# Kernel optimization log

Hardware: AMD Instinct MI355X
Metric: run time of the kernel (lower is better)

The kernel has to match this reference:

```python
import jax, jax.numpy as jnp
import numpy as np

D_MODEL = 1024
NUM_HEADS = 16
D_K = D_MODEL // NUM_HEADS


def setup_inputs() -> dict:
    key = jax.random.key(0)
    ks = jax.random.split(key, 12)
    B, S, D = 2, 2048, D_MODEL
    s = 1.0 / np.sqrt(D)
    inp = {
        "Q": jax.random.normal(ks[0], (B, S, D), jnp.float32),
        "K": jax.random.normal(ks[1], (B, S, D), jnp.float32),
        "V": jax.random.normal(ks[2], (B, S, D), jnp.float32),
        "Wq": jax.random.normal(ks[3], (D, D), jnp.float32) * s,
        "bq": jax.random.normal(ks[4], (D,), jnp.float32) * s,
        "Wk": jax.random.normal(ks[5], (D, D), jnp.float32) * s,
        "bk": jax.random.normal(ks[6], (D,), jnp.float32) * s,
        "Wv": jax.random.normal(ks[7], (D, D), jnp.float32) * s,
        "bv": jax.random.normal(ks[8], (D,), jnp.float32) * s,
        "Wo": jax.random.normal(ks[9], (D, D), jnp.float32) * s,
        "bo": jax.random.normal(ks[10], (D,), jnp.float32) * s,
    }
    return inp


def _split_heads(x, B, S):
    # [B, S, D] -> [B, H, S, d_k]
    return x.reshape(B, S, NUM_HEADS, D_K).transpose(0, 2, 1, 3)


def reference(Q, K, V, Wq, bq, Wk, bk, Wv, bv, Wo, bo):
    B, S, D = Q.shape
    # torch nn.Linear: y = x @ W.T + b
    q = _split_heads(Q @ Wq.T + bq, B, S)
    k = _split_heads(K @ Wk.T + bk, B, S)
    v = _split_heads(V @ Wv.T + bv, B, S)
    scale = 1.0 / np.sqrt(D_K).astype(np.float32)
    # [B, H, S, S] attention scores (materialized, as in the original)
    scores = jnp.einsum('bhqd,bhkd->bhqk', q, k) * scale
    probs = jax.nn.softmax(scores, axis=-1)
    out = jnp.einsum('bhqk,bhkd->bhqd', probs, v)
    out = out.transpose(0, 2, 1, 3).reshape(B, S, D)
    return out @ Wo.T + bo
```

## Files before the change

### kernel.cpp

```cpp
#include <hip/hip_runtime.h>
#include <hip/hip_bf16.h>

#define S_LEN   2048
#define NHEADS  16
#define DKH     64
#define DMODEL  1024
#define NBATCH  2

typedef __bf16 bf16x8 __attribute__((ext_vector_type(8)));
typedef __bf16 bf16x4 __attribute__((ext_vector_type(4)));
typedef float  f32x4  __attribute__((ext_vector_type(4)));

typedef __attribute__((address_space(3))) void       lds_void;
typedef const __attribute__((address_space(1))) void glob_void;

__device__ __forceinline__ void glds16(const void* g, void* l) {
    __builtin_amdgcn_global_load_lds((glob_void*)g, (lds_void*)l, 16, 0, 0);
}

struct CvtArgs {
    const float* src[7];
    __bf16*      dst[7];
    int          n[7];
};

__global__ __launch_bounds__(256)
void cvt_all_k(CvtArgs a)
{
    const int t = blockIdx.y;
    const size_t i = ((size_t)blockIdx.x * 256 + threadIdx.x) * 8;
    if ((int)i >= a.n[t]) return;
    const float* s = a.src[t];
    f32x4 lo = *(const f32x4*)(s + i);
    f32x4 hi = *(const f32x4*)(s + i + 4);
    bf16x8 r;
#pragma unroll
    for (int k = 0; k < 4; ++k) { r[k] = (__bf16)lo[k]; r[4 + k] = (__bf16)hi[k]; }
    *(bf16x8*)(a.dst[t] + i) = r;
}

__device__ __forceinline__ void gemm_core(
    const __bf16* __restrict__ A, const __bf16* __restrict__ W,
    int m0, int n0, int K,
    __bf16 (*As)[32], __bf16 (*Ws)[32], f32x4 acc[4][4])
{
    const int tid  = threadIdx.x;
    const int lane = tid & 63;
    const int wv   = tid >> 6;
    const int l15  = lane & 15;
    const int quad = lane >> 4;
    const int wm   = wv >> 1;
    const int wn   = wv & 1;
    const int grow = lane >> 2;
    const int gcol = (lane & 3) * 8;

    const __bf16* ag0 = A + (size_t)(m0 + wv * 32 + grow) * K + gcol;
    const __bf16* ag1 = A + (size_t)(m0 + wv * 32 + 16 + grow) * K + gcol;
    const __bf16* wg0 = W + (size_t)(n0 + wv * 32 + grow) * K + gcol;
    const __bf16* wg1 = W + (size_t)(n0 + wv * 32 + 16 + grow) * K + gcol;
    void* al0 = &As[wv * 32][0];
    void* al1 = &As[wv * 32 + 16][0];
    void* wl0 = &Ws[wv * 32][0];
    void* wl1 = &Ws[wv * 32 + 16][0];

    for (int k0 = 0;;) {
        __syncthreads();
        glds16(ag0 + k0, al0);
        glds16(ag1 + k0, al1);
        glds16(wg0 + k0, wl0);
        glds16(wg1 + k0, wl1);
        __syncthreads();

        bf16x8 af[4], wf[4];
#pragma unroll
        for (int i = 0; i < 4; ++i)
            af[i] = *(const bf16x8*)&As[wm * 64 + i * 16 + l15][quad * 8];
#pragma unroll
        for (int j = 0; j < 4; ++j)
            wf[j] = *(const bf16x8*)&Ws[wn * 64 + j * 16 + l15][quad * 8];
#pragma unroll
        for (int i = 0; i < 4; ++i)
#pragma unroll
            for (int j = 0; j < 4; ++j)
                acc[i][j] = __builtin_amdgcn_mfma_f32_16x16x32_bf16(af[i], wf[j], acc[i][j], 0, 0, 0);

        k0 += 32;
        if (k0 >= K) break;
    }
}

struct GArgs {
    const __bf16* A[3];
    const __bf16* W[3];
    const float*  bias[3];
    __bf16*       out[3];
};

__global__ __launch_bounds__(256)
void gemm_qkv(GArgs g, int z_off)
{
    __shared__ __align__(16) __bf16 As[128][32];
    __shared__ __align__(16) __bf16 Ws[128][32];

    const int fid = blockIdx.x;
    const int z   = (fid >> 8) + z_off;
    const int f8  = fid & 255;
    int m0, n0;
    if (z == 2) { m0 = (f8 & 7) * 128;  n0 = (f8 >> 3) * 128; }
    else        { m0 = (f8 & 31) * 128; n0 = (f8 >> 5) * 128; }

    f32x4 acc[4][4];
#pragma unroll
    for (int i = 0; i < 4; ++i)
#pragma unroll
        for (int j = 0; j < 4; ++j) acc[i][j] = (f32x4){0.f, 0.f, 0.f, 0.f};

    gemm_core(g.A[z], g.W[z], m0, n0, DMODEL, As, Ws, acc);

    const int lane = threadIdx.x & 63;
    const int wv   = threadIdx.x >> 6;
    const int l15  = lane & 15;
    const int quad = lane >> 4;
    const int wm   = wv >> 1;
    const int wn   = wv & 1;
    const float* bias = g.bias[z];
    __bf16* out = g.out[z];
    const float oscale = (z == 0) ? 0.125f * 1.44269504088896f : 1.0f;

#pragma unroll
    for (int j = 0; j < 4; ++j) {
        const int col = n0 + wn * 64 + j * 16 + l15;
        const float bcol = (z == 2) ? 0.f : bias[col];
#pragma unroll
        for (int i = 0; i < 4; ++i) {
#pragma unroll
            for (int r = 0; r < 4; ++r) {
                const int row = m0 + wm * 64 + i * 16 + quad * 4 + r;
                size_t idx;
                float v = acc[i][j][r];
                if (z == 2) {
                    const int h = row >> 6, d = row & (DKH - 1);
                    const int b = col >> 11, s = col & (S_LEN - 1);
                    v += bias[row];
                    idx = ((size_t)(b * NHEADS + h) * DKH + d) * S_LEN + s;
                } else {
                    const int b = row >> 11, s = row & (S_LEN - 1);
                    const int h = col >> 6, d = col & (DKH - 1);
                    v = (v + bcol) * oscale;
                    idx = ((size_t)(b * NHEADS + h) * S_LEN + s) * DKH + d;
                }
                out[idx] = (__bf16)v;
            }
        }
    }
}

__global__ __launch_bounds__(256)
void gemm_out(const __bf16* __restrict__ A, const __bf16* __restrict__ W,
              const float* __restrict__ bias, float* __restrict__ out)
{
    __shared__ __align__(16) __bf16 As[128][32];
    __shared__ __align__(16) __bf16 Ws[128][32];

    const int fid = blockIdx.x;
    const int m0 = (fid & 31) * 128;
    const int n0 = (fid >> 5) * 128;

    f32x4 acc[4][4];
#pragma unroll
    for (int i = 0; i < 4; ++i)
#pragma unroll
        for (int j = 0; j < 4; ++j) acc[i][j] = (f32x4){0.f, 0.f, 0.f, 0.f};

    gemm_core(A, W, m0, n0, DMODEL, As, Ws, acc);

    const int lane = threadIdx.x & 63;
    const int wv   = threadIdx.x >> 6;
    const int l15  = lane & 15;
    const int quad = lane >> 4;
    const int wm   = wv >> 1;
    const int wn   = wv & 1;

#pragma unroll
    for (int j = 0; j < 4; ++j) {
        const int col = n0 + wn * 64 + j * 16 + l15;
        const float bv = bias[col];
#pragma unroll
        for (int i = 0; i < 4; ++i)
#pragma unroll
            for (int r = 0; r < 4; ++r) {
                const int row = m0 + wm * 64 + i * 16 + quad * 4 + r;
                out[(size_t)row * DMODEL + col] = acc[i][j][r] + bv;
            }
    }
}

__global__ __launch_bounds__(256, 2)
void attn_k(const __bf16* __restrict__ Qh, const __bf16* __restrict__ Kh,
            const __bf16* __restrict__ VhT, __bf16* __restrict__ out,
            float* __restrict__ opart, float* __restrict__ lpart, int ksplit)
{
    __shared__ __align__(16) __bf16 Ks[2][128][64];
    __shared__ __align__(16) __bf16 Vs[64][136];

    const int tid  = threadIdx.x;
    const int lane = tid & 63;
    const int wv   = tid >> 6;
    const int l15  = lane & 15;
    const int quad = lane >> 4;

    const int fid  = blockIdx.x;
    const int x    = fid & 7;
    const int j    = fid >> 3;
    const int bh   = x * 4 + (j & 3);
    const int rest = j >> 2;
    const int q0   = (rest & 7) * 256;
    const int kh   = rest >> 3;
    const int klen = S_LEN / ksplit;
    const int kbeg = kh * klen;
    const int b  = bh >> 4;
    const int h  = bh & (NHEADS - 1);

    const __bf16* Q  = Qh  + (size_t)bh * S_LEN * DKH;
    const __bf16* Kp = Kh  + (size_t)bh * S_LEN * DKH;
    const __bf16* Vt = VhT + (size_t)bh * DKH * S_LEN;

    const int qr0 = q0 + wv * 64 + l15;
    bf16x8 qf[4][2];
#pragma unroll
    for (int s = 0; s < 4; ++s) {
        qf[s][0] = *(const bf16x8*)(Q + (size_t)(qr0 + s * 16) * DKH + quad * 8);
        qf[s][1] = *(const bf16x8*)(Q + (size_t)(qr0 + s * 16) * DKH + quad * 8 + 32);
    }

    const int srow = lane >> 3;
    const int scol = ((lane & 7) ^ srow) << 3;
    char* const ksbase = (char*)&Ks[0][0][0];
    const __bf16* kg[4];
    int kdst[4];
#pragma unroll
    for (int i = 0; i < 4; ++i) {
        const int r = wv * 8 + i * 32 + srow;
        kg[i]   = Kp + (size_t)r * DKH + scol;
        kdst[i] = (wv * 8 + i * 32) * 128;
    }

    const int vrow = tid >> 2;
    const int vc0  = (tid & 3) * 32;
    const __bf16* vst = Vt + (size_t)vrow * S_LEN + vc0;

    f32x4 o[4][4];
#pragma unroll
    for (int s = 0; s < 4; ++s)
#pragma unroll
        for (int jt = 0; jt < 4; ++jt) o[s][jt] = (f32x4){0.f, 0.f, 0.f, 0.f};
    float lacc[4] = {0.f, 0.f, 0.f, 0.f};

    int koff = 0;
#pragma unroll
    for (int i = 0; i < 4; ++i) glds16(kg[i] + (size_t)kbeg * DKH, ksbase + kdst[i]);
    bf16x8 vr[4];
#pragma unroll
    for (int i = 0; i < 4; ++i) vr[i] = *(const bf16x8*)(vst + kbeg + 8 * i);

    for (int kt = kbeg; kt < kbeg + klen; kt += 128) {
        __syncthreads();
#pragma unroll
        for (int i = 0; i < 4; ++i) *(bf16x8*)&Vs[vrow][vc0 + 8 * i] = vr[i];
        __syncthreads();
        if (kt + 128 < kbeg + klen) {
#pragma unroll
            for (int i = 0; i < 4; ++i)
                glds16(kg[i] + (size_t)(kt + 128) * DKH, ksbase + (koff ^ 16384) + kdst[i]);
#pragma unroll
            for (int i = 0; i < 4; ++i)
                vr[i] = *(const bf16x8*)(vst + (kt + 128) + 8 * i);
        }

#pragma unroll
        for (int ht = 0; ht < 2; ++ht) {
            __builtin_amdgcn_s_setprio(1);
            bf16x8 pf[4][2];
#pragma unroll
            for (int tp = 0; tp < 2; ++tp) {
                float p[4][2][4];
#pragma unroll
                for (int ni = 0; ni < 2; ++ni) {
                    const int row = ht * 64 + (tp * 2 + ni) * 16 + l15;
                    const char* kb = ksbase + koff + row * 128;
                    const int sw = (row & 7) << 4;
                    bf16x8 kA = *(const bf16x8*)(kb + ((quad << 4) ^ sw));
                    bf16x8 kB = *(const bf16x8*)(kb + (((quad << 4) + 64) ^ sw));
                    f32x4 s0 = {0.f, 0.f, 0.f, 0.f};
                    f32x4 s1 = {0.f, 0.f, 0.f, 0.f};
                    f32x4 s2 = {0.f, 0.f, 0.f, 0.f};
                    f32x4 s3 = {0.f, 0.f, 0.f, 0.f};
                    s0 = __builtin_amdgcn_mfma_f32_16x16x32_bf16(kA, qf[0][0], s0, 0, 0, 0);
                    s1 = __builtin_amdgcn_mfma_f32_16x16x32_bf16(kA, qf[1][0], s1, 0, 0, 0);
                    s2 = __builtin_amdgcn_mfma_f32_16x16x32_bf16(kA, qf[2][0], s2, 0, 0, 0);
                    s3 = __builtin_amdgcn_mfma_f32_16x16x32_bf16(kA, qf[3][0], s3, 0, 0, 0);
                    s0 = __builtin_amdgcn_mfma_f32_16x16x32_bf16(kB, qf[0][1], s0, 0, 0, 0);
                    s1 = __builtin_amdgcn_mfma_f32_16x16x32_bf16(kB, qf[1][1], s1, 0, 0, 0);
                    s2 = __builtin_amdgcn_mfma_f32_16x16x32_bf16(kB, qf[2][1], s2, 0, 0, 0);
                    s3 = __builtin_amdgcn_mfma_f32_16x16x32_bf16(kB, qf[3][1], s3, 0, 0, 0);
#pragma unroll
                    for (int r = 0; r < 4; ++r) {
                        p[0][ni][r] = __builtin_amdgcn_exp2f(s0[r]);
                        p[1][ni][r] = __builtin_amdgcn_exp2f(s1[r]);
                        p[2][ni][r] = __builtin_amdgcn_exp2f(s2[r]);
                        p[3][ni][r] = __builtin_amdgcn_exp2f(s3[r]);
                    }
                }
#pragma unroll
                for (int s = 0; s < 4; ++s) {
#pragma unroll
                    for (int r = 0; r < 4; ++r) lacc[s] += p[s][0][r] + p[s][1][r];
#pragma unroll
                    for (int jj = 0; jj < 4; ++jj) {
                        pf[s][tp][jj]     = (__bf16)p[s][0][jj];
                        pf[s][tp][4 + jj] = (__bf16)p[s][1][jj];
                    }
                }
            }

#pragma unroll
            for (int t = 0; t < 2; ++t) {
#pragma unroll
                for (int jt = 0; jt < 4; ++jt) {
                    bf16x4 v0 = *(const bf16x4*)&Vs[jt * 16 + l15][ht * 64 + t * 32 + quad * 4];
                    bf16x4 v1 = *(const bf16x4*)&Vs[jt * 16 + l15][ht * 64 + t * 32 + 16 + quad * 4];
                    bf16x8 vf;
#pragma unroll
                    for (int jj = 0; jj < 4; ++jj) { vf[jj] = v0[jj]; vf[4 + jj] = v1[jj]; }
                    o[0][jt] = __builtin_amdgcn_mfma_f32_16x16x32_bf16(vf, pf[0][t], o[0][jt], 0, 0, 0);
                    o[1][jt] = __builtin_amdgcn_mfma_f32_16x16x32_bf16(vf, pf[1][t], o[1][jt], 0, 0, 0);
                    o[2][jt] = __builtin_amdgcn_mfma_f32_16x16x32_bf16(vf, pf[2][t], o[2][jt], 0, 0, 0);
                    o[3][jt] = __builtin_amdgcn_mfma_f32_16x16x32_bf16(vf, pf[3][t], o[3][jt], 0, 0, 0);
                }
            }
            __builtin_amdgcn_s_setprio(0);
        }
        koff ^= 16384;
    }

#pragma unroll
    for (int s = 0; s < 4; ++s) {
        lacc[s] += __shfl_xor(lacc[s], 16);
        lacc[s] += __shfl_xor(lacc[s], 32);
    }

    if (ksplit == 1) {
#pragma unroll
        for (int s = 0; s < 4; ++s) {
            const float inv = 1.0f / lacc[s];
            __bf16* op = out + ((size_t)b * S_LEN + qr0 + s * 16) * DMODEL + h * DKH;
#pragma unroll
            for (int jt = 0; jt < 4; ++jt) {
                bf16x4 tb;
#pragma unroll
                for (int r = 0; r < 4; ++r) tb[r] = (__bf16)(o[s][jt][r] * inv);
                *(bf16x4*)(op + jt * 16 + quad * 4) = tb;
            }
        }
    } else {
#pragma unroll
        for (int s = 0; s < 4; ++s) {
            float* pa = opart + ((size_t)(kh * 32 + bh) * S_LEN + qr0 + s * 16) * DKH;
#pragma unroll
            for (int jt = 0; jt < 4; ++jt)
                *(f32x4*)(pa + jt * 16 + quad * 4) = o[s][jt];
            if (quad == 0)
                lpart[(size_t)(kh * 32 + bh) * S_LEN + qr0 + s * 16] = lacc[s];
        }
    }
}

__global__ __launch_bounds__(256)
void attn_combine(const float* __restrict__ opart, const float* __restrict__ lpart,
                  __bf16* __restrict__ out)
{
    const int t  = blockIdx.x * 256 + threadIdx.x;
    const int d8 = t & 7;
    const int s  = (t >> 3) & (S_LEN - 1);
    const int bh = t >> 14;
    const size_t half = (size_t)32 * S_LEN * DKH;
    const size_t base = ((size_t)bh * S_LEN + s) * DKH + d8 * 8;
    f32x4 a0 = *(const f32x4*)(opart + base);
    f32x4 a1 = *(const f32x4*)(opart + base + 4);
    f32x4 b0 = *(const f32x4*)(opart + base + half);
    f32x4 b1 = *(const f32x4*)(opart + base + half + 4);
    const float inv = 1.0f / (lpart[(size_t)bh * S_LEN + s]
                            + lpart[(size_t)(32 + bh) * S_LEN + s]);
    bf16x8 r;
#pragma unroll
    for (int k = 0; k < 4; ++k) {
        r[k]     = (__bf16)((a0[k] + b0[k]) * inv);
        r[4 + k] = (__bf16)((a1[k] + b1[k]) * inv);
    }
    const int bb = bh >> 4, hh = bh & (NHEADS - 1);
    *(bf16x8*)(out + ((size_t)bb * S_LEN + s) * DMODEL + hh * DKH + d8 * 8) = r;
}

extern "C" void kernel_launch(void* const* d_in, const int* in_sizes, int n_in,
                              void* d_out, int out_size, void* d_ws, size_t ws_size,
                              hipStream_t stream) {
    const float* Qi = (const float*)d_in[0];
    const float* Ki = (const float*)d_in[1];
    const float* Vi = (const float*)d_in[2];
    const float* Wq = (const float*)d_in[3];
    const float* bq = (const float*)d_in[4];
    const float* Wk = (const float*)d_in[5];
    const float* bk = (const float*)d_in[6];
    const float* Wv = (const float*)d_in[7];
    const float* bv = (const float*)d_in[8];
    const float* Wo = (const float*)d_in[9];
    const float* bo = (const float*)d_in[10];
    float* out = (float*)d_out;

    const int M = NBATCH * S_LEN;
    const size_t NW = (size_t)DMODEL * DMODEL;
    const size_t NE = (size_t)M * DMODEL;
    const size_t MB = (size_t)1 << 20;

    __bf16* w_bf   = (__bf16*)d_ws;
    __bf16* q_ws   = w_bf + 4 * NW;
    __bf16* k_ws   = q_ws + NE;
    __bf16* vT_big = k_ws + NE;
    __bf16* Qin_bf = vT_big + NE;
    __bf16* Kin_bf = Qin_bf + NE;
    __bf16* Vin_bf = Kin_bf + NE;
    float*  opart  = (float*)Qin_bf;
    float*  lpart  = (float*)((char*)d_ws + 64 * MB);
    __bf16* attn2  = (__bf16*)((char*)d_ws + 65 * MB);

    const bool big   = ws_size >= 56 * MB;
    const int ksplit = (ws_size >= 73 * MB) ? 2 : 1;
    __bf16* vT_ws   = big ? vT_big : Kin_bf;
    __bf16* attn_ws = (ksplit == 2) ? attn2 : Qin_bf;
    __bf16* wq_bf = w_bf, *wk_bf = w_bf + NW, *wv_bf = w_bf + 2 * NW, *wo_bf = w_bf + 3 * NW;

    CvtArgs ca;
    ca.src[0] = Wq; ca.src[1] = Wk; ca.src[2] = Wv; ca.src[3] = Wo;
    ca.src[4] = Qi; ca.src[5] = Ki; ca.src[6] = Vi;
    ca.dst[0] = wq_bf; ca.dst[1] = wk_bf; ca.dst[2] = wv_bf; ca.dst[3] = wo_bf;
    ca.dst[4] = Qin_bf; ca.dst[5] = Kin_bf; ca.dst[6] = Vin_bf;
    for (int t = 0; t < 4; ++t) ca.n[t] = (int)NW;
    for (int t = 4; t < 7; ++t) ca.n[t] = (int)NE;
    cvt_all_k<<<dim3(2048, 7), 256, 0, stream>>>(ca);

    GArgs g;
    g.A[0] = Qin_bf; g.W[0] = wq_bf; g.bias[0] = bq; g.out[0] = q_ws;
    g.A[1] = Kin_bf; g.W[1] = wk_bf; g.bias[1] = bk; g.out[1] = k_ws;
    g.A[2] = wv_bf;  g.W[2] = Vin_bf; g.bias[2] = bv; g.out[2] = vT_ws;
    if (big) {
        gemm_qkv<<<dim3(768), 256, 0, stream>>>(g, 0);
    } else {
        gemm_qkv<<<dim3(512), 256, 0, stream>>>(g, 0);
        gemm_qkv<<<dim3(256), 256, 0, stream>>>(g, 2);
    }

    attn_k<<<dim3(256 * ksplit), dim3(256), 0, stream>>>(q_ws, k_ws, vT_ws, attn_ws,
                                                         opart, lpart, ksplit);
    if (ksplit == 2)
        attn_combine<<<dim3(2048), 256, 0, stream>>>(opart, lpart, attn_ws);

    gemm_out<<<dim3(256), 256, 0, stream>>>(attn_ws, wo_bf, bo, out);
}
```

Baseline: 230.8 us.

## Fuse fp32-to-bf16 conversion into GEMMs and attention combine into output projection

Removes the standalone conversion kernel: the QKV and output-projection GEMMs now load fp32 inputs and weights straight into LDS with an XOR swizzle and convert to bf16 as fragments are read. The separate attention-combine kernel is folded into the output GEMM, which sums the two split-K partials and normalises while staging the A tile. This saves two launches and the bf16 intermediate traffic, but doubles LDS bytes per tile, adds conversion ALU work in the inner loop, and has the output GEMM re-read the partials for every N tile.

```diff
diff --git a/kernel.cpp b/kernel.cpp
--- a/kernel.cpp
+++ b/kernel.cpp
@@ -18,31 +18,10 @@
     __builtin_amdgcn_global_load_lds((glob_void*)g, (lds_void*)l, 16, 0, 0);
 }
 
-struct CvtArgs {
-    const float* src[7];
-    __bf16*      dst[7];
-    int          n[7];
-};
-
-__global__ __launch_bounds__(256)
-void cvt_all_k(CvtArgs a)
-{
-    const int t = blockIdx.y;
-    const size_t i = ((size_t)blockIdx.x * 256 + threadIdx.x) * 8;
-    if ((int)i >= a.n[t]) return;
-    const float* s = a.src[t];
-    f32x4 lo = *(const f32x4*)(s + i);
-    f32x4 hi = *(const f32x4*)(s + i + 4);
-    bf16x8 r;
-#pragma unroll
-    for (int k = 0; k < 4; ++k) { r[k] = (__bf16)lo[k]; r[4 + k] = (__bf16)hi[k]; }
-    *(bf16x8*)(a.dst[t] + i) = r;
-}
-
-__device__ __forceinline__ void gemm_core(
-    const __bf16* __restrict__ A, const __bf16* __restrict__ W,
+__device__ __forceinline__ void gemm_core_f32(
+    const float* __restrict__ A, const float* __restrict__ W,
     int m0, int n0, int K,
-    __bf16 (*As)[32], __bf16 (*Ws)[32], f32x4 acc[4][4])
+    float (*As)[32], float (*Ws)[32], f32x4 acc[4][4])
 {
     const int tid  = threadIdx.x;
     const int lane = tid & 63;
@@ -51,33 +30,47 @@
     const int quad = lane >> 4;
     const int wm   = wv >> 1;
     const int wn   = wv & 1;
-    const int grow = lane >> 2;
-    const int gcol = (lane & 3) * 8;
-
-    const __bf16* ag0 = A + (size_t)(m0 + wv * 32 + grow) * K + gcol;
-    const __bf16* ag1 = A + (size_t)(m0 + wv * 32 + 16 + grow) * K + gcol;
-    const __bf16* wg0 = W + (size_t)(n0 + wv * 32 + grow) * K + gcol;
-    const __bf16* wg1 = W + (size_t)(n0 + wv * 32 + 16 + grow) * K + gcol;
-    void* al0 = &As[wv * 32][0];
-    void* al1 = &As[wv * 32 + 16][0];
-    void* wl0 = &Ws[wv * 32][0];
-    void* wl1 = &Ws[wv * 32 + 16][0];
+    const int srow = lane >> 3;
+    const int sc   = ((lane & 7) ^ srow) << 2;
+
+    const float* ag[4]; const float* wg[4];
+    void* al[4]; void* wl[4];
+#pragma unroll
+    for (int i = 0; i < 4; ++i) {
+        const int r0 = wv * 8 + i * 32;
+        ag[i] = A + (size_t)(m0 + r0 + srow) * K + sc;
+        wg[i] = W + (size_t)(n0 + r0 + srow) * K + sc;
+        al[i] = &As[r0][0];
+        wl[i] = &Ws[r0][0];
+    }
 
     for (int k0 = 0;;) {
         __syncthreads();
-        glds16(ag0 + k0, al0);
-        glds16(ag1 + k0, al1);
-        glds16(wg0 + k0, wl0);
-        glds16(wg1 + k0, wl1);
+#pragma unroll
+        for (int i = 0; i < 4; ++i) { glds16(ag[i] + k0, al[i]); glds16(wg[i] + k0, wl[i]); }
         __syncthreads();
 
         bf16x8 af[4], wf[4];
 #pragma unroll
-        for (int i = 0; i < 4; ++i)
-            af[i] = *(const bf16x8*)&As[wm * 64 + i * 16 + l15][quad * 8];
-#pragma unroll
-        for (int j = 0; j < 4; ++j)
-            wf[j] = *(const bf16x8*)&Ws[wn * 64 + j * 16 + l15][quad * 8];
+        for (int i = 0; i < 4; ++i) {
+            const int row = wm * 64 + i * 16 + l15;
+            const char* base = (const char*)&As[row][0];
+            const int sw = row & 7;
+            f32x4 lo = *(const f32x4*)(base + (((2 * quad)     ^ sw) << 4));
+            f32x4 hi = *(const f32x4*)(base + (((2 * quad + 1) ^ sw) << 4));
+#pragma unroll
+            for (int j = 0; j < 4; ++j) { af[i][j] = (__bf16)lo[j]; af[i][4 + j] = (__bf16)hi[j]; }
+        }
+#pragma unroll
+        for (int j4 = 0; j4 < 4; ++j4) {
+            const int row = wn * 64 + j4 * 16 + l15;
+            const char* base = (const char*)&Ws[row][0];
+            const int sw = row & 7;
+            f32x4 lo = *(const f32x4*)(base + (((2 * quad)     ^ sw) << 4));
+            f32x4 hi = *(const f32x4*)(base + (((2 * quad + 1) ^ sw) << 4));
+#pragma unroll
+            for (int j = 0; j < 4; ++j) { wf[j4][j] = (__bf16)lo[j]; wf[j4][4 + j] = (__bf16)hi[j]; }
+        }
 #pragma unroll
         for (int i = 0; i < 4; ++i)
 #pragma unroll
@@ -90,20 +83,20 @@
 }
 
 struct GArgs {
-    const __bf16* A[3];
-    const __bf16* W[3];
-    const float*  bias[3];
-    __bf16*       out[3];
+    const float* A[3];
+    const float* W[3];
+    const float* bias[3];
+    __bf16*      out[3];
 };
 
 __global__ __launch_bounds__(256)
-void gemm_qkv(GArgs g, int z_off)
+void gemm_qkv(GArgs g)
 {
-    __shared__ __align__(16) __bf16 As[128][32];
-    __shared__ __align__(16) __bf16 Ws[128][32];
+    __shared__ __align__(16) float As[128][32];
+    __shared__ __align__(16) float Ws[128][32];
 
     const int fid = blockIdx.x;
-    const int z   = (fid >> 8) + z_off;
+    const int z   = fid >> 8;
     const int f8  = fid & 255;
     int m0, n0;
     if (z == 2) { m0 = (f8 & 7) * 128;  n0 = (f8 >> 3) * 128; }
@@ -115,7 +108,7 @@
 #pragma unroll
         for (int j = 0; j < 4; ++j) acc[i][j] = (f32x4){0.f, 0.f, 0.f, 0.f};
 
-    gemm_core(g.A[z], g.W[z], m0, n0, DMODEL, As, Ws, acc);
+    gemm_core_f32(g.A[z], g.W[z], m0, n0, DMODEL, As, Ws, acc);
 
     const int lane = threadIdx.x & 63;
     const int wv   = threadIdx.x >> 6;
@@ -156,30 +149,128 @@
 }
 
 __global__ __launch_bounds__(256)
-void gemm_out(const __bf16* __restrict__ A, const __bf16* __restrict__ W,
-              const float* __restrict__ bias, float* __restrict__ out)
+void gemm_out2(const float* __restrict__ opart, const float* __restrict__ lpart,
+               const __bf16* __restrict__ abf, const float* __restrict__ Wo,
+               const float* __restrict__ bias, float* __restrict__ out, int fused)
 {
-    __shared__ __align__(16) __bf16 As[128][32];
-    __shared__ __align__(16) __bf16 Ws[128][32];
-
-    const int fid = blockIdx.x;
-    const int m0 = (fid & 31) * 128;
-    const int n0 = (fid >> 5) * 128;
-
-    f32x4 acc[4][4];
-#pragma unroll
-    for (int i = 0; i < 4; ++i)
-#pragma unroll
-        for (int j = 0; j < 4; ++j) acc[i][j] = (f32x4){0.f, 0.f, 0.f, 0.f};
-
-    gemm_core(A, W, m0, n0, DMODEL, As, Ws, acc);
-
-    const int lane = threadIdx.x & 63;
-    const int wv   = threadIdx.x >> 6;
+    __shared__ __align__(16) __bf16 As[128][40];
+    __shared__ __align__(16) float  Ws[128][32];
+
+    const int tid  = threadIdx.x;
+    const int lane = tid & 63;
+    const int wv   = tid >> 6;
     const int l15  = lane & 15;
     const int quad = lane >> 4;
     const int wm   = wv >> 1;
     const int wn   = wv & 1;
+    const int fid = blockIdx.x;
+    const int m0 = (fid & 31) * 128;
+    const int n0 = (fid >> 5) * 128;
+
+    const int srow = lane >> 3;
+    const int sc   = ((lane & 7) ^ srow) << 2;
+    const float* wg[4]; void* wl[4];
+#pragma unroll
+    for (int i = 0; i < 4; ++i) {
+        const int r0 = wv * 8 + i * 32;
+        wg[i] = Wo + (size_t)(n0 + r0 + srow) * DMODEL + sc;
+        wl[i] = &Ws[r0][0];
+    }
+
+    const int arow = tid >> 1;
+    const int ac   = (tid & 1) << 4;
+    const int grow = m0 + arow;
+    const int b    = grow >> 11;
+    const int s    = grow & (S_LEN - 1);
+    const size_t halfo = (size_t)32 * S_LEN * DKH;
+
+    f32x4 acc[4][4];
+#pragma unroll
+    for (int i = 0; i < 4; ++i)
+#pragma unroll
+        for (int j = 0; j < 4; ++j) acc[i][j] = (f32x4){0.f, 0.f, 0.f, 0.f};
+
+    f32x4 x[4], y[4];
+    float l0 = 0.f, l1 = 0.f;
+    bf16x8 r0v, r1v;
+
+    {
+        const int gcol = ac;
+        if (fused) {
+            const int h = gcol >> 6;
+            const size_t ba = ((size_t)(b * NHEADS + h) * S_LEN + s) * DKH + (gcol & (DKH - 1));
+#pragma unroll
+            for (int i = 0; i < 4; ++i) { x[i] = *(const f32x4*)(opart + ba + 4 * i);
+                                          y[i] = *(const f32x4*)(opart + halfo + ba + 4 * i); }
+            l0 = lpart[(size_t)(b * NHEADS + h) * S_LEN + s];
+            l1 = lpart[(size_t)(32 + b * NHEADS + h) * S_LEN + s];
+        } else {
+            r0v = *(const bf16x8*)(abf + (size_t)grow * DMODEL + gcol);
+            r1v = *(const bf16x8*)(abf + (size_t)grow * DMODEL + gcol + 8);
+        }
+    }
+
+    for (int k0 = 0;;) {
+        __syncthreads();
+#pragma unroll
+        for (int i = 0; i < 4; ++i) glds16(wg[i] + k0, wl[i]);
+        if (fused) {
+            const float inv = 1.0f / (l0 + l1);
+            bf16x8 w0, w1;
+#pragma unroll
+            for (int j = 0; j < 4; ++j) {
+                w0[j]     = (__bf16)((x[0][j] + y[0][j]) * inv);
+                w0[4 + j] = (__bf16)((x[1][j] + y[1][j]) * inv);
+                w1[j]     = (__bf16)((x[2][j] + y[2][j]) * inv);
+                w1[4 + j] = (__bf16)((x[3][j] + y[3][j]) * inv);
+            }
+            *(bf16x8*)&As[arow][ac]     = w0;
+            *(bf16x8*)&As[arow][ac + 8] = w1;
+        } else {
+            *(bf16x8*)&As[arow][ac]     = r0v;
+            *(bf16x8*)&As[arow][ac + 8] = r1v;
+        }
+        __syncthreads();
+
+        if (k0 + 32 < DMODEL) {
+            const int gcol = k0 + 32 + ac;
+            if (fused) {
+                const int h = gcol >> 6;
+                const size_t ba = ((size_t)(b * NHEADS + h) * S_LEN + s) * DKH + (gcol & (DKH - 1));
+#pragma unroll
+                for (int i = 0; i < 4; ++i) { x[i] = *(const f32x4*)(opart + ba + 4 * i);
+                                              y[i] = *(const f32x4*)(opart + halfo + ba + 4 * i); }
+                l0 = lpart[(size_t)(b * NHEADS + h) * S_LEN + s];
+                l1 = lpart[(size_t)(32 + b * NHEADS + h) * S_LEN + s];
+            } else {
+                r0v = *(const bf16x8*)(abf + (size_t)grow * DMODEL + gcol);
+                r1v = *(const bf16x8*)(abf + (size_t)grow * DMODEL + gcol + 8);
+            }
+        }
+
+        bf16x8 af[4], wf[4];
+#pragma unroll
+        for (int i = 0; i < 4; ++i)
+            af[i] = *(const bf16x8*)&As[wm * 64 + i * 16 + l15][quad * 8];
+#pragma unroll
+        for (int j4 = 0; j4 < 4; ++j4) {
+            const int row = wn * 64 + j4 * 16 + l15;
+            const char* base = (const char*)&Ws[row][0];
+            const int sw = row & 7;
+            f32x4 lo = *(const f32x4*)(base + (((2 * quad)     ^ sw) << 4));
+            f32x4 hi = *(const f32x4*)(base + (((2 * quad + 1) ^ sw) << 4));
+#pragma unroll
+            for (int j = 0; j < 4; ++j) { wf[j4][j] = (__bf16)lo[j]; wf[j4][4 + j] = (__bf16)hi[j]; }
+        }
+#pragma unroll
+        for (int i = 0; i < 4; ++i)
+#pragma unroll
+            for (int j = 0; j < 4; ++j)
+                acc[i][j] = __builtin_amdgcn_mfma_f32_16x16x32_bf16(af[i], wf[j], acc[i][j], 0, 0, 0);
+
+        k0 += 32;
+        if (k0 >= DMODEL) break;
+    }
 
 #pragma unroll
     for (int j = 0; j < 4; ++j) {
@@ -375,32 +466,6 @@
     }
 }
 
-__global__ __launch_bounds__(256)
-void attn_combine(const float* __restrict__ opart, const float* __restrict__ lpart,
-                  __bf16* __restrict__ out)
-{
-    const int t  = blockIdx.x * 256 + threadIdx.x;
-    const int d8 = t & 7;
-    const int s  = (t >> 3) & (S_LEN - 1);
-    const int bh = t >> 14;
-    const size_t half = (size_t)32 * S_LEN * DKH;
-    const size_t base = ((size_t)bh * S_LEN + s) * DKH + d8 * 8;
-    f32x4 a0 = *(const f32x4*)(opart + base);
-    f32x4 a1 = *(const f32x4*)(opart + base + 4);
-    f32x4 b0 = *(const f32x4*)(opart + base + half);
-    f32x4 b1 = *(const f32x4*)(opart + base + half + 4);
-    const float inv = 1.0f / (lpart[(size_t)bh * S_LEN + s]
-                            + lpart[(size_t)(32 + bh) * S_LEN + s]);
-    bf16x8 r;
-#pragma unroll
-    for (int k = 0; k < 4; ++k) {
-        r[k]     = (__bf16)((a0[k] + b0[k]) * inv);
-        r[4 + k] = (__bf16)((a1[k] + b1[k]) * inv);
-    }
-    const int bb = bh >> 4, hh = bh & (NHEADS - 1);
-    *(bf16x8*)(out + ((size_t)bb * S_LEN + s) * DMODEL + hh * DKH + d8 * 8) = r;
-}
-
 extern "C" void kernel_launch(void* const* d_in, const int* in_sizes, int n_in,
                               void* d_out, int out_size, void* d_ws, size_t ws_size,
                               hipStream_t stream) {
@@ -417,52 +482,27 @@
     const float* bo = (const float*)d_in[10];
     float* out = (float*)d_out;
 
-    const int M = NBATCH * S_LEN;
-    const size_t NW = (size_t)DMODEL * DMODEL;
-    const size_t NE = (size_t)M * DMODEL;
+    const size_t NE = (size_t)NBATCH * S_LEN * DMODEL;
     const size_t MB = (size_t)1 << 20;
 
-    __bf16* w_bf   = (__bf16*)d_ws;
-    __bf16* q_ws   = w_bf + 4 * NW;
-    __bf16* k_ws   = q_ws + NE;
-    __bf16* vT_big = k_ws + NE;
-    __bf16* Qin_bf = vT_big + NE;
-    __bf16* Kin_bf = Qin_bf + NE;
-    __bf16* Vin_bf = Kin_bf + NE;
-    float*  opart  = (float*)Qin_bf;
-    float*  lpart  = (float*)((char*)d_ws + 64 * MB);
-    __bf16* attn2  = (__bf16*)((char*)d_ws + 65 * MB);
-
-    const bool big   = ws_size >= 56 * MB;
-    const int ksplit = (ws_size >= 73 * MB) ? 2 : 1;
-    __bf16* vT_ws   = big ? vT_big : Kin_bf;
-    __bf16* attn_ws = (ksplit == 2) ? attn2 : Qin_bf;
-    __bf16* wq_bf = w_bf, *wk_bf = w_bf + NW, *wv_bf = w_bf + 2 * NW, *wo_bf = w_bf + 3 * NW;
-
-    CvtArgs ca;
-    ca.src[0] = Wq; ca.src[1] = Wk; ca.src[2] = Wv; ca.src[3] = Wo;
-    ca.src[4] = Qi; ca.src[5] = Ki; ca.src[6] = Vi;
-    ca.dst[0] = wq_bf; ca.dst[1] = wk_bf; ca.dst[2] = wv_bf; ca.dst[3] = wo_bf;
-    ca.dst[4] = Qin_bf; ca.dst[5] = Kin_bf; ca.dst[6] = Vin_bf;
-    for (int t = 0; t < 4; ++t) ca.n[t] = (int)NW;
-    for (int t = 4; t < 7; ++t) ca.n[t] = (int)NE;
-    cvt_all_k<<<dim3(2048, 7), 256, 0, stream>>>(ca);
+    __bf16* q_ws  = (__bf16*)d_ws;
+    __bf16* k_ws  = q_ws + NE;
+    __bf16* vT_ws = k_ws + NE;
+    float*  opart = (float*)((char*)d_ws + 24 * MB);
+    float*  lpart = (float*)((char*)d_ws + 56 * MB);
+    __bf16* attn1 = (__bf16*)((char*)d_ws + 24 * MB);
+
+    const int ksplit = (ws_size >= 57 * MB) ? 2 : 1;
 
     GArgs g;
-    g.A[0] = Qin_bf; g.W[0] = wq_bf; g.bias[0] = bq; g.out[0] = q_ws;
-    g.A[1] = Kin_bf; g.W[1] = wk_bf; g.bias[1] = bk; g.out[1] = k_ws;
-    g.A[2] = wv_bf;  g.W[2] = Vin_bf; g.bias[2] = bv; g.out[2] = vT_ws;
-    if (big) {
-        gemm_qkv<<<dim3(768), 256, 0, stream>>>(g, 0);
-    } else {
-        gemm_qkv<<<dim3(512), 256, 0, stream>>>(g, 0);
-        gemm_qkv<<<dim3(256), 256, 0, stream>>>(g, 2);
-    }
-
-    attn_k<<<dim3(256 * ksplit), dim3(256), 0, stream>>>(q_ws, k_ws, vT_ws, attn_ws,
+    g.A[0] = Qi; g.W[0] = Wq; g.bias[0] = bq; g.out[0] = q_ws;
+    g.A[1] = Ki; g.W[1] = Wk; g.bias[1] = bk; g.out[1] = k_ws;
+    g.A[2] = Wv; g.W[2] = Vi; g.bias[2] = bv; g.out[2] = vT_ws;
+    gemm_qkv<<<dim3(768), 256, 0, stream>>>(g);
+
+    attn_k<<<dim3(256 * ksplit), dim3(256), 0, stream>>>(q_ws, k_ws, vT_ws, attn1,
                                                          opart, lpart, ksplit);
-    if (ksplit == 2)
-        attn_combine<<<dim3(2048), 256, 0, stream>>>(opart, lpart, attn_ws);
-
-    gemm_out<<<dim3(256), 256, 0, stream>>>(attn_ws, wo_bf, bo, out);
+
+    gemm_out2<<<dim3(256), 256, 0, stream>>>(opart, lpart, attn1, Wo, bo, out,
+                                             ksplit == 2);
 }
```

Measured after the change: 285.9 us. 1.24x slower.
